# Performance work log

Measured on AMD Instinct MI355X. Metric: run time of the kernel, lower is better.

The kernel has to match this reference:

```python
import jax, jax.numpy as jnp
import numpy as np

N_NODE = 40000  # item vocabulary
H = 100         # hidden size (SR-GNN default)
B = 64          # sessions per batch
L = 16          # items per session (equal-length sessions)
N = B * L       # total graph nodes
E = 2048        # total edges
NL = 1          # GatedGraphConv layers


def setup_inputs() -> dict:
    key = jax.random.key(0)
    ks = jax.random.split(key, 20)
    stdv = 1.0 / np.sqrt(H)
    u = lambda k, shape: jax.random.uniform(k, shape, jnp.float32, -stdv, stdv)
    return {
        "x": jax.random.randint(ks[0], (N,), 0, N_NODE),
        "edge_index": jax.random.randint(ks[1], (2, E), 0, N),
        "edge_weight": jax.random.uniform(ks[2], (E,), jnp.float32),
        "batch": jnp.arange(N) // L,  # node -> session id, equal-length sessions
        "embed": u(ks[3], (N_NODE, H)),
        "ggc_w": u(ks[4], (NL, H, H)),
        "gru_wih": u(ks[5], (3 * H, H)),
        "gru_whh": u(ks[6], (3 * H, H)),
        "gru_bih": u(ks[7], (3 * H,)),
        "gru_bhh": u(ks[8], (3 * H,)),
        "W1_w": u(ks[9], (H, H)), "W1_b": u(ks[10], (H,)),
        "W2_w": u(ks[11], (H, H)), "W2_b": u(ks[12], (H,)),
        "Wt_w": u(ks[13], (H, H)), "Wt_b": u(ks[14], (H,)),
        "q_w": u(ks[15], (1, H)), "q_b": u(ks[16], (1,)),
        "W3_w": u(ks[17], (H, 2 * H)), "W3_b": u(ks[18], (H,)),
    }


def reference(x, edge_index, edge_weight, batch, embed, ggc_w, gru_wih, gru_whh,
              gru_bih, gru_bhh, W1_w, W1_b, W2_w, W2_b, Wt_w, Wt_b, q_w, q_b,
              W3_w, W3_b):
    # Embedding lookup
    h = embed[x]  # [N, H]
    src, dst = edge_index[0], edge_index[1]
    # GatedGraphConv: weighted message aggregation + GRUCell update
    for l in range(NL):
        m = h @ ggc_w[l]                                             # [N, H]
        agg = jnp.zeros_like(h).at[dst].add(edge_weight[:, None] * m[src])
        gi = agg @ gru_wih.T + gru_bih                               # [N, 3H]
        gh = h @ gru_whh.T + gru_bhh
        ir, iz, inn = jnp.split(gi, 3, axis=-1)
        hr, hz, hn = jnp.split(gh, 3, axis=-1)
        r = jax.nn.sigmoid(ir + hr)
        zg = jax.nn.sigmoid(iz + hz)
        ng = jnp.tanh(inn + r * hn)
        h = (1.0 - zg) * ng + zg * h
    v = h.reshape(B, L, H)                                           # sessions
    s_l = v[:, -1]                                                   # [B, H] last item
    # alpha = q(sigmoid(W1(v_n) + W2(v)))
    a = jax.nn.sigmoid((s_l @ W1_w.T + W1_b)[:, None, :] + (v @ W2_w.T + W2_b))
    alpha = a @ q_w.T + q_b                                          # [B, L, 1]
    s_g = jnp.sum(alpha * v, axis=1)                                 # [B, H]
    s_h = jnp.concatenate([s_l, s_g], axis=-1) @ W3_w.T + W3_b       # [B, H]
    # Target attention: s_t[b] = softmax(E @ W_t(v_b)^T, -1) @ v_b, contracted
    # directly against E to avoid materializing [B, N_NODE, H].
    vt = v @ Wt_w.T + Wt_b                                           # [B, L, H]
    P = jax.nn.softmax(jnp.einsum('jh,blh->bjl', embed, vt), axis=-1)
    C = jnp.einsum('blh,jh->bjl', v, embed)                          # v_l . E_j
    z = s_h @ embed.T + jnp.sum(P * C, axis=-1)                      # [B, N_NODE]
    return z
```

## Files before the change

kernel.cpp:

```cpp
#include <hip/hip_runtime.h>
#include <hip/hip_bf16.h>

#define Hh    100
#define NN    1024
#define BB    64
#define LL    16
#define EE    2048
#define NNODE 40000

#define BSPL  8
#define BPB   (BB / BSPL)
#define PFR   12
#define PPAN  (PFR * 64 * 8)

typedef unsigned short u16;
typedef __attribute__((ext_vector_type(8))) short short8;
typedef __attribute__((ext_vector_type(4))) float f32x4;

__device__ __forceinline__ float bf2f(u16 u) {
    union { unsigned int i; float f; } v;
    v.i = ((unsigned int)u) << 16;
    return v.f;
}

__device__ __forceinline__ u16 f2bf(float f) {
    unsigned int x = __float_as_uint(f);
    unsigned int lsb = (x >> 16) & 1u;
    x += 0x7fffu + lsb;
    return (u16)(x >> 16);
}

__device__ __forceinline__ float sigmoidf_(float x) {
    return 1.0f / (1.0f + expf(-x));
}

template <bool BF>
__device__ __forceinline__ float ldv(const void* p, size_t i) {
    if (BF) return bf2f(((const u16*)p)[i]);
    return ((const float*)p)[i];
}
__device__ __forceinline__ float ldvf(int flag, const void* p, size_t i) {
    return flag ? ldv<true>(p, i) : ldv<false>(p, i);
}

template <bool BF>
__device__ void cvt_impl(int t,
                         const void* ew, const void* ggc, const void* wih, const void* whh,
                         const void* bih, const void* bhh, const void* W1w, const void* W1b,
                         const void* W2w, const void* W2b, const void* Wtw, const void* Wtb,
                         const void* qw, const void* qb, const void* W3w, const void* W3b,
                         float* __restrict__ W) {
    const void* src; int si; int doff; int di;
    if      (t <   2048) { src = ew;  si = t;          doff = 0;      di = si; }
    else if (t <  12048) { src = ggc; si = t - 2048;   doff = 2048;   di = si; }
    else if (t <  42048) { src = wih; si = t - 12048;  doff = 12048;  di = (si % 100) * 300 + si / 100; }
    else if (t <  72048) { src = whh; si = t - 42048;  doff = 42048;  di = (si % 100) * 300 + si / 100; }
    else if (t <  72348) { src = bih; si = t - 72048;  doff = 72048;  di = si; }
    else if (t <  72648) { src = bhh; si = t - 72348;  doff = 72352;  di = si; }
    else if (t <  82648) { src = W1w; si = t - 72648;  doff = 72656;  di = (si % 100) * 100 + si / 100; }
    else if (t <  82748) { src = W1b; si = t - 82648;  doff = 82656;  di = si; }
    else if (t <  92748) { src = W2w; si = t - 82748;  doff = 82768;  di = (si % 100) * 100 + si / 100; }
    else if (t <  92848) { src = W2b; si = t - 92748;  doff = 92768;  di = si; }
    else if (t < 102848) { src = Wtw; si = t - 92848;  doff = 92880;  di = (si % 100) * 100 + si / 100; }
    else if (t < 102948) { src = Wtb; si = t - 102848; doff = 102880; di = si; }
    else if (t < 103048) { src = qw;  si = t - 102948; doff = 102992; di = si; }
    else if (t < 103049) { src = qb;  si = t - 103048; doff = 103104; di = si; }
    else if (t < 123049) { src = W3w; si = t - 103049; doff = 103120; di = (si % 200) * 100 + si / 200; }
    else                 { src = W3b; si = t - 123049; doff = 123120; di = si; }
    W[doff + di] = ldv<BF>(src, si);
}

__global__ void __launch_bounds__(256) k_cvt(const void* embed_raw, int* __restrict__ flag,
                      const void* ew, const void* ggc, const void* wih, const void* whh,
                      const void* bih, const void* bhh, const void* W1w, const void* W1b,
                      const void* W2w, const void* W2b, const void* Wtw, const void* Wtb,
                      const void* qw, const void* qb, const void* W3w, const void* W3b,
                      float* __restrict__ W) {
    __shared__ int cnt;
    if (threadIdx.x == 0) cnt = 0;
    __syncthreads();
    int bad = 0;
    const u16* eb = (const u16*)embed_raw;
    for (int i = threadIdx.x; i < 4096; i += 256) {
        float v = bf2f(eb[i]);
        if (!(fabsf(v) <= 0.5f)) bad++;
    }
    if (bad) atomicAdd(&cnt, bad);
    __syncthreads();
    const bool bf = (cnt == 0);
    if (blockIdx.x == 0 && threadIdx.x == 0) flag[0] = bf ? 1 : 0;
    int t = blockIdx.x * 256 + threadIdx.x;
    if (t >= 123149) return;
    if (bf) cvt_impl<true >(t, ew, ggc, wih, whh, bih, bhh, W1w, W1b, W2w, W2b, Wtw, Wtb, qw, qb, W3w, W3b, W);
    else    cvt_impl<false>(t, ew, ggc, wih, whh, bih, bhh, W1w, W1b, W2w, W2b, Wtw, Wtb, qw, qb, W3w, W3b, W);
}

__global__ void __launch_bounds__(256) k_gm(const int* __restrict__ flag,
                                            const int* __restrict__ x,
                                            const void* __restrict__ embed,
                                            const float* __restrict__ ggc_w,
                                            float* __restrict__ m,
                                            float* __restrict__ agg) {
    __shared__ float W[Hh * Hh];
    __shared__ float H[8 * Hh];
    const int tid = threadIdx.x;
    const int fl = flag[0];
    const int r0 = blockIdx.x * 8;
    for (int idx = tid; idx < Hh * Hh; idx += 256) W[idx] = ggc_w[idx];
    for (int idx = tid; idx < 8 * Hh; idx += 256) {
        int i = idx / Hh, j = idx - i * Hh;
        H[idx] = ldvf(fl, embed, (size_t)x[r0 + i] * Hh + j);
    }
    for (int idx = tid; idx < 8 * Hh; idx += 256) agg[r0 * Hh + idx] = 0.0f;
    __syncthreads();
    for (int idx = tid; idx < 8 * Hh; idx += 256) {
        int i = idx / Hh, j = idx - i * Hh;
        float acc = 0.0f;
#pragma unroll 4
        for (int k = 0; k < Hh; ++k) acc += H[i * Hh + k] * W[k * Hh + j];
        m[(r0 + i) * Hh + j] = acc;
    }
}

__global__ void k_scatter(const int* __restrict__ ei, const float* __restrict__ ew,
                          const float* __restrict__ m, float* __restrict__ agg) {
    int t = blockIdx.x * 256 + threadIdx.x;
    if (t >= EE * Hh) return;
    int e = t / Hh, j = t - e * Hh;
    int src = ei[e], dst = ei[EE + e];
    atomicAdd(&agg[dst * Hh + j], ew[e] * m[src * Hh + j]);
}

__global__ void k_gru(const int* __restrict__ flag, const int* __restrict__ x,
                      const void* __restrict__ embed,
                      const float* __restrict__ agg,
                      const float* __restrict__ wihT, const float* __restrict__ whhT,
                      const float* __restrict__ bih, const float* __restrict__ bhh,
                      float* __restrict__ h1) {
    int t = blockIdx.x * 256 + threadIdx.x;
    if (t >= NN * Hh) return;
    int i = t / Hh, j = t - i * Hh;
    const int fl = flag[0];
    const size_t erow = (size_t)x[i] * Hh;
    const float* ar = agg + i * Hh;
    float s_ir = bih[j], s_iz = bih[j + Hh], s_in = bih[j + 2 * Hh];
    float s_hr = bhh[j], s_hz = bhh[j + Hh], s_hn = bhh[j + 2 * Hh];
    float h0j = 0.0f;
    for (int k = 0; k < Hh; ++k) {
        float a = ar[k];
        float h = ldvf(fl, embed, erow + k);
        if (k == j) h0j = h;
        const float* wT = wihT + k * 300;
        const float* uT = whhT + k * 300;
        s_ir += a * wT[j];
        s_iz += a * wT[j + 100];
        s_in += a * wT[j + 200];
        s_hr += h * uT[j];
        s_hz += h * uT[j + 100];
        s_hn += h * uT[j + 200];
    }
    float r = sigmoidf_(s_ir + s_hr);
    float z = sigmoidf_(s_iz + s_hz);
    float n = tanhf(s_in + r * s_hn);
    h1[t] = (1.0f - z) * n + z * h0j;
}

__global__ void __launch_bounds__(256) k_att(const float* __restrict__ h1,
                    const float* __restrict__ W1T, const float* __restrict__ W1b,
                    const float* __restrict__ W2T, const float* __restrict__ W2b,
                    const float* __restrict__ WtT, const float* __restrict__ Wtb,
                    const float* __restrict__ qw, const float* __restrict__ qb,
                    const float* __restrict__ W3T, const float* __restrict__ W3b,
                    u16* __restrict__ P) {
    __shared__ float V[LL * Hh];
    __shared__ float Q2[LL * Hh];
    __shared__ float VTs[LL * Hh];
    __shared__ float Q1[Hh];
    __shared__ float AL[LL];
    __shared__ float SG[Hh];
    __shared__ float SH[Hh];
    const int b = blockIdx.x, tid = threadIdx.x;
    for (int idx = tid; idx < LL * Hh; idx += 256) V[idx] = h1[b * LL * Hh + idx];
    __syncthreads();
    for (int idx = tid; idx < LL * Hh; idx += 256) {
        int i = idx / Hh, j = idx - i * Hh;
        float a2 = 0, at = 0;
        for (int k = 0; k < Hh; ++k) {
            float vk = V[i * Hh + k];
            a2 += vk * W2T[k * Hh + j];
            at += vk * WtT[k * Hh + j];
        }
        Q2[idx] = a2 + W2b[j];
        VTs[idx] = at + Wtb[j];
    }
    if (tid < Hh) {
        float a1 = 0;
        for (int k = 0; k < Hh; ++k) a1 += V[(LL - 1) * Hh + k] * W1T[k * Hh + tid];
        Q1[tid] = a1 + W1b[tid];
    }
    __syncthreads();
    if (tid < LL) {
        float acc = 0;
        for (int j = 0; j < Hh; ++j)
            acc += sigmoidf_(Q1[j] + Q2[tid * Hh + j]) * qw[j];
        AL[tid] = acc + qb[0];
    }
    __syncthreads();
    if (tid < Hh) {
        float acc = 0;
#pragma unroll
        for (int l = 0; l < LL; ++l) acc += AL[l] * V[l * Hh + tid];
        SG[tid] = acc;
    }
    __syncthreads();
    if (tid < Hh) {
        float acc = W3b[tid];
        for (int k = 0; k < Hh; ++k) acc += V[(LL - 1) * Hh + k] * W3T[k * Hh + tid];
        for (int k = 0; k < Hh; ++k) acc += SG[k] * W3T[(Hh + k) * Hh + tid];
        SH[tid] = acc;
    }
    __syncthreads();
    for (int w = tid; w < PFR * 64; w += 256) {
        int f = w >> 6, lane = w & 63;
        int t = f >> 2, ks = f & 3;
        int mm = lane & 15, qq = lane >> 4;
        int row = t * 16 + mm;
        int col0 = ks * 32 + qq * 8;
        short8 t8;
#pragma unroll
        for (int e = 0; e < 8; ++e) {
            int col = col0 + e;
            float v = 0.0f;
            if (col < Hh) {
                if      (row < 16) v = VTs[row * Hh + col];
                else if (row < 32) v = V[(row - 16) * Hh + col];
                else if (row == 32) v = SH[col];
            }
            t8[e] = (short)f2bf(v);
        }
        *(short8*)&P[((size_t)b * PFR + f) * 512 + lane * 8] = t8;
    }
}

__device__ __forceinline__ short8 load_efrag(const void* embed, bool bf, int j, int k0) {
    short8 v = {0, 0, 0, 0, 0, 0, 0, 0};
    if (j >= NNODE || k0 >= Hh) return v;
    if (bf) {
        const u16* row = (const u16*)embed + (size_t)j * Hh + k0;
        if (k0 + 8 <= Hh) {
            ushort4 a = *(const ushort4*)(row);
            ushort4 b = *(const ushort4*)(row + 4);
            v[0] = (short)a.x; v[1] = (short)a.y; v[2] = (short)a.z; v[3] = (short)a.w;
            v[4] = (short)b.x; v[5] = (short)b.y; v[6] = (short)b.z; v[7] = (short)b.w;
        } else {
            for (int e = 0; e < Hh - k0; ++e) v[e] = (short)row[e];
        }
    } else {
        const float* row = (const float*)embed + (size_t)j * Hh + k0;
        if (k0 + 8 <= Hh) {
            float4 a = *(const float4*)(row);
            float4 b = *(const float4*)(row + 4);
            v[0] = (short)f2bf(a.x); v[1] = (short)f2bf(a.y); v[2] = (short)f2bf(a.z); v[3] = (short)f2bf(a.w);
            v[4] = (short)f2bf(b.x); v[5] = (short)f2bf(b.y); v[6] = (short)f2bf(b.z); v[7] = (short)f2bf(b.w);
        } else {
            for (int e = 0; e < Hh - k0; ++e) v[e] = (short)f2bf(row[e]);
        }
    }
    return v;
}

__global__ void __launch_bounds__(256) k_score(const int* __restrict__ flag,
                                               const void* __restrict__ embed,
                                               const u16* __restrict__ P,
                                               void* __restrict__ out) {
    __shared__ alignas(16) u16 sPan[2][PPAN];
    const int jb = blockIdx.x * 128;
    const int b0 = blockIdx.y * BPB;
    const int tid = threadIdx.x;
    const bool bf = (flag[0] != 0);
    const int wave = tid >> 6, lane = tid & 63;
    const int m = lane & 15, quad = lane >> 4;

    short8 Bf[2][4];
#pragma unroll
    for (int g = 0; g < 2; ++g)
#pragma unroll
        for (int ks = 0; ks < 4; ++ks)
            Bf[g][ks] = load_efrag(embed, bf, jb + wave * 32 + g * 16 + m, ks * 32 + quad * 8);

    short8 pa = {0, 0, 0, 0, 0, 0, 0, 0};
    short8 pb = {0, 0, 0, 0, 0, 0, 0, 0};
    if (quad == 0) {
        pa[0] = (short)f2bf((float)m);
        pb[0] = (short)f2bf(1.0f);
    }
    f32x4 pd = (f32x4){0.0f, 0.0f, 0.0f, 0.0f};
    pd = __builtin_amdgcn_mfma_f32_16x16x32_bf16(pa, pb, pd, 0, 0, 0);
    const bool isH1 =
        (__builtin_amdgcn_readfirstlane(__float_as_uint(pd[1])) == 0x3f800000u);

    {
        const uint4* s4 = (const uint4*)(P + (size_t)b0 * PPAN);
        uint4 g0 = s4[tid], g1 = s4[tid + 256], g2 = s4[tid + 512];
        uint4* d = (uint4*)sPan[0];
        d[tid] = g0; d[tid + 256] = g1; d[tid + 512] = g2;
    }
    __syncthreads();

    int cur = 0;
    for (int bi = 0; bi < BPB; ++bi) {
        const int b = b0 + bi;
        uint4 g0, g1, g2;
        if (bi + 1 < BPB) {
            const uint4* s4 = (const uint4*)(P + (size_t)(b + 1) * PPAN);
            g0 = s4[tid]; g1 = s4[tid + 256]; g2 = s4[tid + 512];
        }

        const u16* sp = sPan[cur];
        f32x4 acc[2][3];
#pragma unroll
        for (int g = 0; g < 2; ++g)
#pragma unroll
            for (int t = 0; t < 3; ++t)
                acc[g][t] = (f32x4){0.0f, 0.0f, 0.0f, 0.0f};
#pragma unroll
        for (int t = 0; t < 3; ++t) {
            short8 A0 = *(const short8*)&sp[(t * 4 + 0) * 512 + lane * 8];
            short8 A1 = *(const short8*)&sp[(t * 4 + 1) * 512 + lane * 8];
            short8 A2 = *(const short8*)&sp[(t * 4 + 2) * 512 + lane * 8];
            short8 A3 = *(const short8*)&sp[(t * 4 + 3) * 512 + lane * 8];
#pragma unroll
            for (int g = 0; g < 2; ++g) {
                acc[g][t] = __builtin_amdgcn_mfma_f32_16x16x32_bf16(A0, Bf[g][0], acc[g][t], 0, 0, 0);
                acc[g][t] = __builtin_amdgcn_mfma_f32_16x16x32_bf16(A1, Bf[g][1], acc[g][t], 0, 0, 0);
                acc[g][t] = __builtin_amdgcn_mfma_f32_16x16x32_bf16(A2, Bf[g][2], acc[g][t], 0, 0, 0);
                acc[g][t] = __builtin_amdgcn_mfma_f32_16x16x32_bf16(A3, Bf[g][3], acc[g][t], 0, 0, 0);
            }
        }

#pragma unroll
        for (int g = 0; g < 2; ++g) {
            if (isH1) {
                float den = 0.0f, num = 0.0f;
#pragma unroll
                for (int r = 0; r < 4; ++r) {
                    float p = __expf(acc[g][0][r]);
                    den += p;
                    num += p * acc[g][1][r];
                }
                den += __shfl_xor(den, 16); num += __shfl_xor(num, 16);
                den += __shfl_xor(den, 32); num += __shfl_xor(num, 32);
                if (quad == 0) {
                    int j = jb + wave * 32 + g * 16 + m;
                    if (j < NNODE) {
                        float z = acc[g][2][0] + num / den;
                        if (bf) ((u16*)out)[(size_t)b * NNODE + j] = f2bf(z);
                        else    ((float*)out)[(size_t)b * NNODE + j] = z;
                    }
                }
            } else {
                float den[4], num[4];
#pragma unroll
                for (int r = 0; r < 4; ++r) {
                    float p = __expf(acc[g][0][r]);
                    den[r] = p;
                    num[r] = p * acc[g][1][r];
                }
#pragma unroll
                for (int s = 1; s <= 8; s <<= 1)
#pragma unroll
                    for (int r = 0; r < 4; ++r) {
                        den[r] += __shfl_xor(den[r], s);
                        num[r] += __shfl_xor(num[r], s);
                    }
                if (m == 0) {
#pragma unroll
                    for (int r = 0; r < 4; ++r) {
                        int j = jb + wave * 32 + g * 16 + quad * 4 + r;
                        if (j < NNODE) {
                            float z = acc[g][2][r] + num[r] / den[r];
                            if (bf) ((u16*)out)[(size_t)b * NNODE + j] = f2bf(z);
                            else    ((float*)out)[(size_t)b * NNODE + j] = z;
                        }
                    }
                }
            }
        }

        if (bi + 1 < BPB) {
            uint4* d = (uint4*)sPan[cur ^ 1];
            d[tid] = g0; d[tid + 256] = g1; d[tid + 512] = g2;
        }
        __syncthreads();
        cur ^= 1;
    }
}

extern "C" void kernel_launch(void* const* d_in, const int* in_sizes, int n_in,
                              void* d_out, int out_size, void* d_ws, size_t ws_size,
                              hipStream_t stream) {
    const int* x      = (const int*)d_in[0];
    const int* ei     = (const int*)d_in[1];
    const void* ew    = d_in[2];
    const void* embed = d_in[4];
    const void* ggc   = d_in[5];
    const void* wih   = d_in[6];
    const void* whh   = d_in[7];
    const void* bih   = d_in[8];
    const void* bhh   = d_in[9];
    const void* W1w   = d_in[10];
    const void* W1b   = d_in[11];
    const void* W2w   = d_in[12];
    const void* W2b   = d_in[13];
    const void* Wtw   = d_in[14];
    const void* Wtb   = d_in[15];
    const void* qw    = d_in[16];
    const void* qb    = d_in[17];
    const void* W3w   = d_in[18];
    const void* W3b   = d_in[19];
    float* ws = (float*)d_ws;
    int* flag = (int*)d_ws;

    float* W = ws + 64;
    float* ew_f  = W + 0;
    float* ggc_f = W + 2048;
    float* wihT  = W + 12048;
    float* whhT  = W + 42048;
    float* bih_f = W + 72048;
    float* bhh_f = W + 72352;
    float* W1T   = W + 72656;
    float* W1b_f = W + 82656;
    float* W2T   = W + 82768;
    float* W2b_f = W + 92768;
    float* WtT   = W + 92880;
    float* Wtb_f = W + 102880;
    float* qw_f  = W + 102992;
    float* qb_f  = W + 103104;
    float* W3T   = W + 103120;
    float* W3b_f = W + 123120;

    float* D     = ws + 123296;
    float* m     = D;
    float* agg   = D + 102400;
    float* h1    = D;
    u16*   P     = (u16*)(D + 102400);

    k_cvt    <<<dim3(482), dim3(256), 0, stream>>>(embed, flag, ew, ggc, wih, whh, bih, bhh,
                                                   W1w, W1b, W2w, W2b, Wtw, Wtb, qw, qb, W3w, W3b, W);
    k_gm     <<<dim3(128), dim3(256), 0, stream>>>(flag, x, embed, ggc_f, m, agg);
    k_scatter<<<dim3(800), dim3(256), 0, stream>>>(ei, ew_f, m, agg);
    k_gru    <<<dim3(400), dim3(256), 0, stream>>>(flag, x, embed, agg, wihT, whhT, bih_f, bhh_f, h1);
    k_att    <<<dim3(64),  dim3(256), 0, stream>>>(h1, W1T, W1b_f, W2T, W2b_f, WtT, Wtb_f,
                                                   qw_f, qb_f, W3T, W3b_f, P);
    k_score  <<<dim3((NNODE + 127) / 128, BSPL), dim3(256), 0, stream>>>(flag, embed, P, d_out);
}
```

Before: 234.8 us.

## Batch s_h·E across sessions, widen score tiles, pre-pack embed to bf16, interleave GRU weights

After: 222.8 us. -5.1%, faster.

```diff
diff --git a/kernel.cpp b/kernel.cpp
--- a/kernel.cpp
+++ b/kernel.cpp
@@ -10,8 +10,10 @@
 
 #define BSPL  8
 #define BPB   (BB / BSPL)
-#define PFR   12
+#define PFR   8
 #define PPAN  (PFR * 64 * 8)
+#define GJ    4
+#define EBS   104
 
 typedef unsigned short u16;
 typedef __attribute__((ext_vector_type(8))) short short8;
@@ -53,20 +55,20 @@
     const void* src; int si; int doff; int di;
     if      (t <   2048) { src = ew;  si = t;          doff = 0;      di = si; }
     else if (t <  12048) { src = ggc; si = t - 2048;   doff = 2048;   di = si; }
-    else if (t <  42048) { src = wih; si = t - 12048;  doff = 12048;  di = (si % 100) * 300 + si / 100; }
-    else if (t <  72048) { src = whh; si = t - 42048;  doff = 42048;  di = (si % 100) * 300 + si / 100; }
-    else if (t <  72348) { src = bih; si = t - 72048;  doff = 72048;  di = si; }
-    else if (t <  72648) { src = bhh; si = t - 72348;  doff = 72352;  di = si; }
-    else if (t <  82648) { src = W1w; si = t - 72648;  doff = 72656;  di = (si % 100) * 100 + si / 100; }
-    else if (t <  82748) { src = W1b; si = t - 82648;  doff = 82656;  di = si; }
-    else if (t <  92748) { src = W2w; si = t - 82748;  doff = 82768;  di = (si % 100) * 100 + si / 100; }
-    else if (t <  92848) { src = W2b; si = t - 92748;  doff = 92768;  di = si; }
-    else if (t < 102848) { src = Wtw; si = t - 92848;  doff = 92880;  di = (si % 100) * 100 + si / 100; }
-    else if (t < 102948) { src = Wtb; si = t - 102848; doff = 102880; di = si; }
-    else if (t < 103048) { src = qw;  si = t - 102948; doff = 102992; di = si; }
-    else if (t < 103049) { src = qb;  si = t - 103048; doff = 103104; di = si; }
-    else if (t < 123049) { src = W3w; si = t - 103049; doff = 103120; di = (si % 200) * 100 + si / 200; }
-    else                 { src = W3b; si = t - 123049; doff = 123120; di = si; }
+    else if (t <  42048) { src = wih; si = t - 12048;  doff = 12048;  { int r = si / 100, k = si - r * 100; di = k * 800 + (r % 100) * 8 + r / 100; } }
+    else if (t <  72048) { src = whh; si = t - 42048;  doff = 12048;  { int r = si / 100, k = si - r * 100; di = k * 800 + (r % 100) * 8 + 3 + r / 100; } }
+    else if (t <  72348) { src = bih; si = t - 72048;  doff = 92048;  di = si; }
+    else if (t <  72648) { src = bhh; si = t - 72348;  doff = 92352;  di = si; }
+    else if (t <  82648) { src = W1w; si = t - 72648;  doff = 92656;  di = (si % 100) * 100 + si / 100; }
+    else if (t <  82748) { src = W1b; si = t - 82648;  doff = 102656; di = si; }
+    else if (t <  92748) { src = W2w; si = t - 82748;  doff = 102768; di = (si % 100) * 100 + si / 100; }
+    else if (t <  92848) { src = W2b; si = t - 92748;  doff = 112768; di = si; }
+    else if (t < 102848) { src = Wtw; si = t - 92848;  doff = 112880; di = (si % 100) * 100 + si / 100; }
+    else if (t < 102948) { src = Wtb; si = t - 102848; doff = 122880; di = si; }
+    else if (t < 103048) { src = qw;  si = t - 102948; doff = 122992; di = si; }
+    else if (t < 103049) { src = qb;  si = t - 103048; doff = 123104; di = si; }
+    else if (t < 123049) { src = W3w; si = t - 103049; doff = 123120; di = (si % 200) * 100 + si / 200; }
+    else                 { src = W3b; si = t - 123049; doff = 143120; di = si; }
     W[doff + di] = ldv<BF>(src, si);
 }
 
@@ -75,7 +77,7 @@
                       const void* bih, const void* bhh, const void* W1w, const void* W1b,
                       const void* W2w, const void* W2b, const void* Wtw, const void* Wtb,
                       const void* qw, const void* qb, const void* W3w, const void* W3b,
-                      float* __restrict__ W) {
+                      float* __restrict__ W, u16* __restrict__ SD) {
     __shared__ int cnt;
     if (threadIdx.x == 0) cnt = 0;
     __syncthreads();
@@ -90,9 +92,31 @@
     const bool bf = (cnt == 0);
     if (blockIdx.x == 0 && threadIdx.x == 0) flag[0] = bf ? 1 : 0;
     int t = blockIdx.x * 256 + threadIdx.x;
+    if (t < 8192) ((unsigned int*)SD)[t] = 0u;
     if (t >= 123149) return;
     if (bf) cvt_impl<true >(t, ew, ggc, wih, whh, bih, bhh, W1w, W1b, W2w, W2b, Wtw, Wtb, qw, qb, W3w, W3b, W);
     else    cvt_impl<false>(t, ew, ggc, wih, whh, bih, bhh, W1w, W1b, W2w, W2b, Wtw, Wtb, qw, qb, W3w, W3b, W);
+}
+
+__global__ void __launch_bounds__(256) k_ecvt(const int* __restrict__ flag,
+                                              const void* __restrict__ embed,
+                                              u16* __restrict__ EB) {
+    const bool bf = (flag[0] != 0);
+    int t = blockIdx.x * 256 + threadIdx.x;
+    const int total = NNODE * (EBS / 2);
+    if (t >= total) return;
+    int r = t / (EBS / 2), c2 = t - r * (EBS / 2);
+    int k0 = c2 * 2;
+    unsigned int w = 0;
+    if (k0 + 1 < Hh) {
+        if (bf) {
+            w = *(const unsigned int*)&((const u16*)embed)[(size_t)r * Hh + k0];
+        } else {
+            float2 e2 = *(const float2*)&((const float*)embed)[(size_t)r * Hh + k0];
+            w = (unsigned int)f2bf(e2.x) | ((unsigned int)f2bf(e2.y) << 16);
+        }
+    }
+    ((unsigned int*)EB)[t] = w;
 }
 
 __global__ void __launch_bounds__(256) k_gm(const int* __restrict__ flag,
@@ -134,7 +158,7 @@
 __global__ void k_gru(const int* __restrict__ flag, const int* __restrict__ x,
                       const void* __restrict__ embed,
                       const float* __restrict__ agg,
-                      const float* __restrict__ wihT, const float* __restrict__ whhT,
+                      const float* __restrict__ wC,
                       const float* __restrict__ bih, const float* __restrict__ bhh,
                       float* __restrict__ h1) {
     int t = blockIdx.x * 256 + threadIdx.x;
@@ -146,18 +170,20 @@
     float s_ir = bih[j], s_iz = bih[j + Hh], s_in = bih[j + 2 * Hh];
     float s_hr = bhh[j], s_hz = bhh[j + Hh], s_hn = bhh[j + 2 * Hh];
     float h0j = 0.0f;
+    const float* wbase = wC + j * 8;
     for (int k = 0; k < Hh; ++k) {
         float a = ar[k];
         float h = ldvf(fl, embed, erow + k);
         if (k == j) h0j = h;
-        const float* wT = wihT + k * 300;
-        const float* uT = whhT + k * 300;
-        s_ir += a * wT[j];
-        s_iz += a * wT[j + 100];
-        s_in += a * wT[j + 200];
-        s_hr += h * uT[j];
-        s_hz += h * uT[j + 100];
-        s_hn += h * uT[j + 200];
+        const float* wr = wbase + k * 800;
+        float4 w0 = *(const float4*)wr;
+        float2 w1 = *(const float2*)(wr + 4);
+        s_ir += a * w0.x;
+        s_iz += a * w0.y;
+        s_in += a * w0.z;
+        s_hr += h * w0.w;
+        s_hz += h * w1.x;
+        s_hn += h * w1.y;
     }
     float r = sigmoidf_(s_ir + s_hr);
     float z = sigmoidf_(s_iz + s_hz);
@@ -171,7 +197,7 @@
                     const float* __restrict__ WtT, const float* __restrict__ Wtb,
                     const float* __restrict__ qw, const float* __restrict__ qb,
                     const float* __restrict__ W3T, const float* __restrict__ W3b,
-                    u16* __restrict__ P) {
+                    u16* __restrict__ P, u16* __restrict__ SD) {
     __shared__ float V[LL * Hh];
     __shared__ float Q2[LL * Hh];
     __shared__ float VTs[LL * Hh];
@@ -224,21 +250,22 @@
         int f = w >> 6, lane = w & 63;
         int t = f >> 2, ks = f & 3;
         int mm = lane & 15, qq = lane >> 4;
-        int row = t * 16 + mm;
         int col0 = ks * 32 + qq * 8;
         short8 t8;
 #pragma unroll
         for (int e = 0; e < 8; ++e) {
             int col = col0 + e;
             float v = 0.0f;
-            if (col < Hh) {
-                if      (row < 16) v = VTs[row * Hh + col];
-                else if (row < 32) v = V[(row - 16) * Hh + col];
-                else if (row == 32) v = SH[col];
-            }
+            if (col < Hh) v = (t == 0) ? VTs[mm * Hh + col] : V[mm * Hh + col];
             t8[e] = (short)f2bf(v);
         }
         *(short8*)&P[((size_t)b * PFR + f) * 512 + lane * 8] = t8;
+    }
+    if (tid < 128) {
+        int ks = tid >> 5, qq = (tid >> 3) & 3, e = tid & 7;
+        int col = ks * 32 + qq * 8 + e;
+        float v = (col < Hh) ? SH[col] : 0.0f;
+        SD[(((size_t)(b >> 3) * 4 + ks) * 64 + qq * 16 + (b & 7)) * 8 + e] = f2bf(v);
     }
 }
 
@@ -269,68 +296,83 @@
     return v;
 }
 
+template <int EMODE>
 __global__ void __launch_bounds__(256) k_score(const int* __restrict__ flag,
                                                const void* __restrict__ embed,
+                                               const u16* __restrict__ EB,
                                                const u16* __restrict__ P,
+                                               const u16* __restrict__ SD,
                                                void* __restrict__ out) {
     __shared__ alignas(16) u16 sPan[2][PPAN];
-    const int jb = blockIdx.x * 128;
+    const int jb = blockIdx.x * 256;
     const int b0 = blockIdx.y * BPB;
+    const int slice = blockIdx.y;
     const int tid = threadIdx.x;
     const bool bf = (flag[0] != 0);
     const int wave = tid >> 6, lane = tid & 63;
     const int m = lane & 15, quad = lane >> 4;
 
-    short8 Bf[2][4];
-#pragma unroll
-    for (int g = 0; g < 2; ++g)
+    short8 Bf[GJ][4];
+#pragma unroll
+    for (int g = 0; g < GJ; ++g)
+#pragma unroll
+        for (int ks = 0; ks < 4; ++ks) {
+            int j = jb + wave * 64 + g * 16 + m;
+            if (EMODE) {
+                short8 v = {0, 0, 0, 0, 0, 0, 0, 0};
+                if (j < NNODE)
+                    v = *(const short8*)&EB[(size_t)j * EBS + ks * 32 + quad * 8];
+                Bf[g][ks] = v;
+            } else {
+                Bf[g][ks] = load_efrag(embed, bf, j, ks * 32 + quad * 8);
+            }
+        }
+
+    short8 Sf[4];
+#pragma unroll
+    for (int ks = 0; ks < 4; ++ks)
+        Sf[ks] = *(const short8*)&SD[(((size_t)slice * 4 + ks) * 64 + lane) * 8];
+    f32x4 accsd[GJ];
+#pragma unroll
+    for (int g = 0; g < GJ; ++g) {
+        accsd[g] = (f32x4){0.0f, 0.0f, 0.0f, 0.0f};
 #pragma unroll
         for (int ks = 0; ks < 4; ++ks)
-            Bf[g][ks] = load_efrag(embed, bf, jb + wave * 32 + g * 16 + m, ks * 32 + quad * 8);
-
-    short8 pa = {0, 0, 0, 0, 0, 0, 0, 0};
-    short8 pb = {0, 0, 0, 0, 0, 0, 0, 0};
-    if (quad == 0) {
-        pa[0] = (short)f2bf((float)m);
-        pb[0] = (short)f2bf(1.0f);
-    }
-    f32x4 pd = (f32x4){0.0f, 0.0f, 0.0f, 0.0f};
-    pd = __builtin_amdgcn_mfma_f32_16x16x32_bf16(pa, pb, pd, 0, 0, 0);
-    const bool isH1 =
-        (__builtin_amdgcn_readfirstlane(__float_as_uint(pd[1])) == 0x3f800000u);
+            accsd[g] = __builtin_amdgcn_mfma_f32_16x16x32_bf16(Sf[ks], Bf[g][ks], accsd[g], 0, 0, 0);
+    }
 
     {
         const uint4* s4 = (const uint4*)(P + (size_t)b0 * PPAN);
-        uint4 g0 = s4[tid], g1 = s4[tid + 256], g2 = s4[tid + 512];
+        uint4 g0 = s4[tid], g1 = s4[tid + 256];
         uint4* d = (uint4*)sPan[0];
-        d[tid] = g0; d[tid + 256] = g1; d[tid + 512] = g2;
+        d[tid] = g0; d[tid + 256] = g1;
     }
     __syncthreads();
 
     int cur = 0;
     for (int bi = 0; bi < BPB; ++bi) {
         const int b = b0 + bi;
-        uint4 g0, g1, g2;
+        uint4 g0, g1;
         if (bi + 1 < BPB) {
             const uint4* s4 = (const uint4*)(P + (size_t)(b + 1) * PPAN);
-            g0 = s4[tid]; g1 = s4[tid + 256]; g2 = s4[tid + 512];
+            g0 = s4[tid]; g1 = s4[tid + 256];
         }
 
         const u16* sp = sPan[cur];
-        f32x4 acc[2][3];
-#pragma unroll
-        for (int g = 0; g < 2; ++g)
-#pragma unroll
-            for (int t = 0; t < 3; ++t)
+        f32x4 acc[GJ][2];
+#pragma unroll
+        for (int g = 0; g < GJ; ++g)
+#pragma unroll
+            for (int t = 0; t < 2; ++t)
                 acc[g][t] = (f32x4){0.0f, 0.0f, 0.0f, 0.0f};
 #pragma unroll
-        for (int t = 0; t < 3; ++t) {
+        for (int t = 0; t < 2; ++t) {
             short8 A0 = *(const short8*)&sp[(t * 4 + 0) * 512 + lane * 8];
             short8 A1 = *(const short8*)&sp[(t * 4 + 1) * 512 + lane * 8];
             short8 A2 = *(const short8*)&sp[(t * 4 + 2) * 512 + lane * 8];
             short8 A3 = *(const short8*)&sp[(t * 4 + 3) * 512 + lane * 8];
 #pragma unroll
-            for (int g = 0; g < 2; ++g) {
+            for (int g = 0; g < GJ; ++g) {
                 acc[g][t] = __builtin_amdgcn_mfma_f32_16x16x32_bf16(A0, Bf[g][0], acc[g][t], 0, 0, 0);
                 acc[g][t] = __builtin_amdgcn_mfma_f32_16x16x32_bf16(A1, Bf[g][1], acc[g][t], 0, 0, 0);
                 acc[g][t] = __builtin_amdgcn_mfma_f32_16x16x32_bf16(A2, Bf[g][2], acc[g][t], 0, 0, 0);
@@ -339,57 +381,33 @@
         }
 
 #pragma unroll
-        for (int g = 0; g < 2; ++g) {
-            if (isH1) {
-                float den = 0.0f, num = 0.0f;
-#pragma unroll
-                for (int r = 0; r < 4; ++r) {
-                    float p = __expf(acc[g][0][r]);
-                    den += p;
-                    num += p * acc[g][1][r];
-                }
-                den += __shfl_xor(den, 16); num += __shfl_xor(num, 16);
-                den += __shfl_xor(den, 32); num += __shfl_xor(num, 32);
-                if (quad == 0) {
-                    int j = jb + wave * 32 + g * 16 + m;
-                    if (j < NNODE) {
-                        float z = acc[g][2][0] + num / den;
-                        if (bf) ((u16*)out)[(size_t)b * NNODE + j] = f2bf(z);
-                        else    ((float*)out)[(size_t)b * NNODE + j] = z;
-                    }
-                }
-            } else {
-                float den[4], num[4];
-#pragma unroll
-                for (int r = 0; r < 4; ++r) {
-                    float p = __expf(acc[g][0][r]);
-                    den[r] = p;
-                    num[r] = p * acc[g][1][r];
-                }
-#pragma unroll
-                for (int s = 1; s <= 8; s <<= 1)
-#pragma unroll
-                    for (int r = 0; r < 4; ++r) {
-                        den[r] += __shfl_xor(den[r], s);
-                        num[r] += __shfl_xor(num[r], s);
-                    }
-                if (m == 0) {
-#pragma unroll
-                    for (int r = 0; r < 4; ++r) {
-                        int j = jb + wave * 32 + g * 16 + quad * 4 + r;
-                        if (j < NNODE) {
-                            float z = acc[g][2][r] + num[r] / den[r];
-                            if (bf) ((u16*)out)[(size_t)b * NNODE + j] = f2bf(z);
-                            else    ((float*)out)[(size_t)b * NNODE + j] = z;
-                        }
-                    }
+        for (int g = 0; g < GJ; ++g) {
+            float den = 0.0f, num = 0.0f;
+#pragma unroll
+            for (int r = 0; r < 4; ++r) {
+                float p = __expf(acc[g][0][r]);
+                den += p;
+                num += p * acc[g][1][r];
+            }
+            den += __shfl_xor(den, 16); num += __shfl_xor(num, 16);
+            den += __shfl_xor(den, 32); num += __shfl_xor(num, 32);
+            f32x4 s4v = accsd[g];
+            int rr = bi & 3;
+            float sdv = (rr == 0) ? s4v[0] : (rr == 1) ? s4v[1] : (rr == 2) ? s4v[2] : s4v[3];
+            sdv = __shfl(sdv, ((bi >> 2) << 4) | m);
+            if (quad == 0) {
+                int j = jb + wave * 64 + g * 16 + m;
+                if (j < NNODE) {
+                    float z = sdv + num / den;
+                    if (bf) ((u16*)out)[(size_t)b * NNODE + j] = f2bf(z);
+                    else    ((float*)out)[(size_t)b * NNODE + j] = z;
                 }
             }
         }
 
         if (bi + 1 < BPB) {
             uint4* d = (uint4*)sPan[cur ^ 1];
-            d[tid] = g0; d[tid + 256] = g1; d[tid + 512] = g2;
+            d[tid] = g0; d[tid + 256] = g1;
         }
         __syncthreads();
         cur ^= 1;
@@ -424,33 +442,42 @@
     float* W = ws + 64;
     float* ew_f  = W + 0;
     float* ggc_f = W + 2048;
-    float* wihT  = W + 12048;
-    float* whhT  = W + 42048;
-    float* bih_f = W + 72048;
-    float* bhh_f = W + 72352;
-    float* W1T   = W + 72656;
-    float* W1b_f = W + 82656;
-    float* W2T   = W + 82768;
-    float* W2b_f = W + 92768;
-    float* WtT   = W + 92880;
-    float* Wtb_f = W + 102880;
-    float* qw_f  = W + 102992;
-    float* qb_f  = W + 103104;
-    float* W3T   = W + 103120;
-    float* W3b_f = W + 123120;
-
-    float* D     = ws + 123296;
+    float* wC    = W + 12048;
+    float* bih_f = W + 92048;
+    float* bhh_f = W + 92352;
+    float* W1T   = W + 92656;
+    float* W1b_f = W + 102656;
+    float* W2T   = W + 102768;
+    float* W2b_f = W + 112768;
+    float* WtT   = W + 112880;
+    float* Wtb_f = W + 122880;
+    float* qw_f  = W + 122992;
+    float* qb_f  = W + 123104;
+    float* W3T   = W + 123120;
+    float* W3b_f = W + 143120;
+
+    float* D     = ws + 143296;
     float* m     = D;
     float* agg   = D + 102400;
     float* h1    = D;
     u16*   P     = (u16*)(D + 102400);
+    u16*   SDp   = (u16*)(D + 233472);
+    u16*   EB    = (u16*)(D + 241664);
+
+    const size_t need_bytes = (size_t)(143296 + 241664) * 4 + (size_t)NNODE * EBS * 2;
+    const bool emode = (ws_size >= need_bytes);
 
     k_cvt    <<<dim3(482), dim3(256), 0, stream>>>(embed, flag, ew, ggc, wih, whh, bih, bhh,
-                                                   W1w, W1b, W2w, W2b, Wtw, Wtb, qw, qb, W3w, W3b, W);
+                                                   W1w, W1b, W2w, W2b, Wtw, Wtb, qw, qb, W3w, W3b, W, SDp);
+    if (emode)
+        k_ecvt<<<dim3((NNODE * (EBS / 2) + 255) / 256), dim3(256), 0, stream>>>(flag, embed, EB);
     k_gm     <<<dim3(128), dim3(256), 0, stream>>>(flag, x, embed, ggc_f, m, agg);
     k_scatter<<<dim3(800), dim3(256), 0, stream>>>(ei, ew_f, m, agg);
-    k_gru    <<<dim3(400), dim3(256), 0, stream>>>(flag, x, embed, agg, wihT, whhT, bih_f, bhh_f, h1);
+    k_gru    <<<dim3(400), dim3(256), 0, stream>>>(flag, x, embed, agg, wC, bih_f, bhh_f, h1);
     k_att    <<<dim3(64),  dim3(256), 0, stream>>>(h1, W1T, W1b_f, W2T, W2b_f, WtT, Wtb_f,
-                                                   qw_f, qb_f, W3T, W3b_f, P);
-    k_score  <<<dim3((NNODE + 127) / 128, BSPL), dim3(256), 0, stream>>>(flag, embed, P, d_out);
-}
+                                                   qw_f, qb_f, W3T, W3b_f, P, SDp);
+    if (emode)
+        k_score<1><<<dim3((NNODE + 255) / 256, BSPL), dim3(256), 0, stream>>>(flag, embed, EB, P, SDp, d_out);
+    else
+        k_score<0><<<dim3((NNODE + 255) / 256, BSPL), dim3(256), 0, stream>>>(flag, embed, EB, P, SDp, d_out);
+}
```
